# Performance work log

Measured on AMD Instinct MI355X. Metric: run time of the kernel, lower is better.

Reference implementation:

```python
import jax, jax.numpy as jnp
import numpy as np

DELTA = 0.5  # fuzziness factor (module default)

def setup_inputs() -> dict:
    key = jax.random.key(0)
    kq, kk, kv = jax.random.split(key, 3)
    B, L, H, E = 2, 2048, 16, 64
    queries = jax.random.normal(kq, (B, L, H, E), jnp.float32)
    keys_ = jax.random.normal(kk, (B, L, H, E), jnp.float32)
    values = jax.random.normal(kv, (B, L, H, E), jnp.float32)
    # TriangularCausalMask: True above the diagonal -> masked out
    attn_mask = jnp.triu(jnp.ones((L, L), dtype=bool), k=1)[None, None]  # [1,1,L,L]
    return {"queries": queries, "keys": keys_, "values": values, "attn_mask": attn_mask}

def reference(queries, keys, values, attn_mask):
    # queries: [B,L,H,E], keys/values: [B,S,H,E], attn_mask: [1,1,L,S] bool (True = masked)
    E = queries.shape[-1]
    scale = 1.0 / np.sqrt(E)
    scores = jnp.einsum('blhe,bshe->bhls', queries, keys)  # [B,H,L,S]
    # fuzzy modification; note sigmoid(-inf)=0 so masking before or after is equivalent,
    # we mask after for grad safety
    fuzzy = scores + DELTA * jax.nn.sigmoid(scores)
    fuzzy = jnp.where(attn_mask, -jnp.inf, fuzzy)
    A = jax.nn.softmax(scale * fuzzy, axis=-1)  # dropout p=0 (eval mode)
    V = jnp.einsum('bhls,bshd->blhd', A, values)  # [B,L,H,D]
    return V
```

## Files before the change

### kernel.cpp

```cpp
#include <hip/hip_runtime.h>
#include <math.h>


typedef __bf16 bf16x8 __attribute__((ext_vector_type(8)));
typedef __bf16 bf16x4 __attribute__((ext_vector_type(4)));
typedef float  f32x4  __attribute__((ext_vector_type(4)));

constexpr int Lc = 2048, Hc = 16, Ec = 64;
constexpr int QBLK = 64, KVB = 64;
constexpr int NQT  = Lc / QBLK;
constexpr int ROWS = Hc * Ec;
constexpr float LOG2E = 1.4426950408889634f;
constexpr float C1 = 0.125f * LOG2E;
constexpr float C3 = 0.5f * 0.125f * LOG2E;

__global__ __launch_bounds__(256)
void conv_kv(const float* __restrict__ Kp, const float* __restrict__ Vp,
             __bf16* __restrict__ Kbf, __bf16* __restrict__ Vbf) {
    const int bid = blockIdx.x;
    const int tid = threadIdx.x;
    if (bid < 1024) {
        const int task = bid * 256 + tid;
        const int row = task >> 2, q4 = task & 3;
        const int h = row & 15, bl = row >> 4;
        const int b = bl >> 11, l = bl & 2047;
        const float4* src = reinterpret_cast<const float4*>(Kp + (size_t)row * 64 + q4 * 16);
        __bf16* dst = Kbf + ((size_t)((b * 16 + h) * 2048 + l)) * 64 + q4 * 16;
        float4 x0 = src[0], x1 = src[1], x2 = src[2], x3 = src[3];
        bf16x8 o0, o1;
        o0[0]=(__bf16)x0.x; o0[1]=(__bf16)x0.y; o0[2]=(__bf16)x0.z; o0[3]=(__bf16)x0.w;
        o0[4]=(__bf16)x1.x; o0[5]=(__bf16)x1.y; o0[6]=(__bf16)x1.z; o0[7]=(__bf16)x1.w;
        o1[0]=(__bf16)x2.x; o1[1]=(__bf16)x2.y; o1[2]=(__bf16)x2.z; o1[3]=(__bf16)x2.w;
        o1[4]=(__bf16)x3.x; o1[5]=(__bf16)x3.y; o1[6]=(__bf16)x3.z; o1[7]=(__bf16)x3.w;
        reinterpret_cast<bf16x8*>(dst)[0] = o0;
        reinterpret_cast<bf16x8*>(dst)[1] = o1;
    } else {
        __shared__ __bf16 tl[64 * 72];
        const int vb = bid - 1024;
        const int bh = vb >> 5, lt = vb & 31;
        const int b = bh >> 4, h = bh & 15;
        {
            const int l = tid >> 2, dc = tid & 3;
            const float4* src = reinterpret_cast<const float4*>(
                Vp + ((size_t)((b * 2048 + lt * 64 + l) * 16 + h)) * 64 + dc * 16);
            float4 v0 = src[0], v1 = src[1], v2 = src[2], v3 = src[3];
            float e[16] = {v0.x,v0.y,v0.z,v0.w, v1.x,v1.y,v1.z,v1.w,
                           v2.x,v2.y,v2.z,v2.w, v3.x,v3.y,v3.z,v3.w};
            #pragma unroll
            for (int i = 0; i < 16; ++i) tl[(dc * 16 + i) * 72 + l] = (__bf16)e[i];
        }
        __syncthreads();
        {
            const int d = tid >> 2, lc = tid & 3;
            bf16x8 a = *reinterpret_cast<const bf16x8*>(&tl[d * 72 + lc * 16]);
            bf16x8 c = *reinterpret_cast<const bf16x8*>(&tl[d * 72 + lc * 16 + 8]);
            __bf16* dst = Vbf + ((size_t)bh * 64 + d) * 2048 + lt * 64 + lc * 16;
            reinterpret_cast<bf16x8*>(dst)[0] = a;
            reinterpret_cast<bf16x8*>(dst)[1] = c;
        }
    }
}

__global__ __launch_bounds__(256, 4)
void fuzzy_attn_mfma(const float* __restrict__ Qp, const __bf16* __restrict__ Kbf,
                     const __bf16* __restrict__ Vbf, float* __restrict__ Op) {
    __shared__ char smem[24576];
    __bf16* kt0 = reinterpret_cast<__bf16*>(smem);
    __bf16* vt0 = reinterpret_cast<__bf16*>(smem + 8192);

    const int id  = blockIdx.x;
    const int xcd = id & 7;
    const int r_  = id >> 3;
    const int s4  = r_ & 3;
    const int j   = r_ >> 2;
    const int jHi = j >> 3, jLo = j & 7;
    int qt;
    if      (jHi == 0) qt = 31 - jLo;
    else if (jHi == 1) qt = jLo;
    else if (jHi == 2) qt = 23 - jLo;
    else               qt = 8 + jLo;
    const int bh  = s4 * 8 + xcd;
    const int b = bh >> 4, h = bh & 15;

    const int tid  = threadIdx.x;
    const int lane = tid & 63;
    const int w    = tid >> 6;
    const int q16  = lane & 15;
    const int g    = lane >> 4;
    const int qhalf  = w & 1;
    const int kvhalf = w >> 1;

    const __bf16* Kh = Kbf + (size_t)bh * (Lc * Ec);
    const __bf16* Vh = Vbf + (size_t)bh * (Ec * Lc);
    const float*  Qb = Qp + (size_t)b * Lc * ROWS + h * Ec;
    float*        Ob = Op + (size_t)b * Lc * ROWS + h * Ec;

    const int qrow0 = qt * QBLK + qhalf * 32 + q16;
    const int qrow1 = qrow0 + 16;

    const int srow0 = w * 8 + (lane >> 3);
    const int srow1 = srow0 + 32;
    const int sch0  = (lane & 7) ^ ((srow0 & 7) ^ (srow0 >> 3));
    const int sch1  = (lane & 7) ^ ((srow1 & 7) ^ (srow1 >> 3));
    const __bf16* kgA = Kh + srow0 * 64   + sch0 * 8;
    const __bf16* kgB = Kh + srow1 * 64   + sch1 * 8;
    const __bf16* vgA = Vh + srow0 * 2048 + sch0 * 8;
    const __bf16* vgB = Vh + srow1 * 2048 + sch1 * 8;

    bf16x8 qb[2][2];
    #pragma unroll
    for (int qs = 0; qs < 2; ++qs) {
        #pragma unroll
        for (int ks = 0; ks < 2; ++ks) {
            const float* qp = Qb + (size_t)(qs ? qrow1 : qrow0) * ROWS + g * 8 + 32 * ks;
            float4 x0 = reinterpret_cast<const float4*>(qp)[0];
            float4 x1 = reinterpret_cast<const float4*>(qp)[1];
            bf16x8 tq;
            tq[0]=(__bf16)x0.x; tq[1]=(__bf16)x0.y; tq[2]=(__bf16)x0.z; tq[3]=(__bf16)x0.w;
            tq[4]=(__bf16)x1.x; tq[5]=(__bf16)x1.y; tq[6]=(__bf16)x1.z; tq[7]=(__bf16)x1.w;
            qb[qs][ks] = tq;
        }
    }

    const int nst = qt + 1;

    #define STAGE_K(st_)                                                              \
        do {                                                                          \
            const __bf16* kga = kgA + (size_t)(st_) * (KVB * Ec);                     \
            const __bf16* kgb = kgB + (size_t)(st_) * (KVB * Ec);                     \
            __builtin_amdgcn_global_load_lds(                                         \
                (const __attribute__((address_space(1))) void*)kga,                   \
                (__attribute__((address_space(3))) void*)&kt0[w * 512], 16, 0, 0);    \
            __builtin_amdgcn_global_load_lds(                                         \
                (const __attribute__((address_space(1))) void*)kgb,                   \
                (__attribute__((address_space(3))) void*)&kt0[2048 + w * 512], 16, 0, 0); \
        } while (0)
    #define STAGE_V(st_)                                                              \
        do {                                                                          \
            const __bf16* vga = vgA + (st_) * KVB;                                    \
            const __bf16* vgb = vgB + (st_) * KVB;                                    \
            __builtin_amdgcn_global_load_lds(                                         \
                (const __attribute__((address_space(1))) void*)vga,                   \
                (__attribute__((address_space(3))) void*)&vt0[w * 512], 16, 0, 0);    \
            __builtin_amdgcn_global_load_lds(                                         \
                (const __attribute__((address_space(1))) void*)vgb,                   \
                (__attribute__((address_space(3))) void*)&vt0[2048 + w * 512], 16, 0, 0); \
        } while (0)

    STAGE_K(0);
    __syncthreads();

    float la0 = 0.f, la1 = 0.f;
    float lb0 = 0.f, lb1 = 0.f;
    f32x4 oacc[2][4];
    #pragma unroll
    for (int qs = 0; qs < 2; ++qs) {
        #pragma unroll
        for (int ds = 0; ds < 4; ++ds) { f32x4 z = {0.f,0.f,0.f,0.f}; oacc[qs][ds] = z; }
    }

    char* pw = smem + 16384 + w * 2048;
    const int pswz = (q16 & 3) ^ ((q16 >> 2) & 3);

    const char* kbase = reinterpret_cast<const char*>(kt0);
    const char* vbase = reinterpret_cast<const char*>(vt0);

    for (int st = 0; st < nst; ++st) {
        STAGE_V(st);

        f32x4 sacc[2][2];
        #pragma unroll
        for (int kv = 0; kv < 2; ++kv) {
            #pragma unroll
            for (int qs = 0; qs < 2; ++qs) { f32x4 z = {0.f,0.f,0.f,0.f}; sacc[kv][qs] = z; }
        }
        __builtin_amdgcn_s_setprio(1);
        #pragma unroll
        for (int kv = 0; kv < 2; ++kv) {
            const int kvr  = kvhalf * 32 + kv * 16 + q16;
            const int kkey = ((kvr & 7) ^ (kvr >> 3)) << 4;
            #pragma unroll
            for (int ks = 0; ks < 2; ++ks) {
                bf16x8 ka = *reinterpret_cast<const bf16x8*>(
                    kbase + kvr * 128 + (((g + 4 * ks) << 4) ^ kkey));
                sacc[kv][0] = __builtin_amdgcn_mfma_f32_16x16x32_bf16(ka, qb[0][ks], sacc[kv][0], 0, 0, 0);
                sacc[kv][1] = __builtin_amdgcn_mfma_f32_16x16x32_bf16(ka, qb[1][ks], sacc[kv][1], 0, 0, 0);
            }
        }
        __builtin_amdgcn_s_setprio(0);

        const bool diagm = (st == qt) && (kvhalf >= qhalf);
        #pragma unroll
        for (int kv = 0; kv < 2; ++kv) {
            #pragma unroll
            for (int qs = 0; qs < 2; ++qs) {
                const int qrow_s = qs ? qrow1 : qrow0;
                float p4[4];
                #pragma unroll
                for (int r = 0; r < 4; ++r) {
                    const float s  = sacc[kv][qs][r];
                    const float sg = __builtin_amdgcn_fmed3f(fmaf(s, 0.1875f, 0.5f), 0.f, 1.f);
                    float u = fmaf(sg, C3, s * C1);
                    if (diagm) {
                        const int kvg = st * KVB + kvhalf * 32 + kv * 16 + 4 * g + r;
                        if (kvg > qrow_s) u = -INFINITY;
                    }
                    p4[r] = __builtin_amdgcn_exp2f(u);
                }
                if (qs == 0) { la0 += p4[0] + p4[1]; la1 += p4[2] + p4[3]; }
                else         { lb0 += p4[0] + p4[1]; lb1 += p4[2] + p4[3]; }
                bf16x4 pk;
                pk[0]=(__bf16)p4[0]; pk[1]=(__bf16)p4[1]; pk[2]=(__bf16)p4[2]; pk[3]=(__bf16)p4[3];
                *reinterpret_cast<bf16x4*>(
                    pw + (qs * 16 + q16) * 64 +
                    (((2 * kv + (g >> 1)) ^ pswz) << 4) + (g & 1) * 8) = pk;
            }
        }

        __syncthreads();

        if (st + 1 < nst) STAGE_K(st + 1);

        bf16x8 pa0 = *reinterpret_cast<const bf16x8*>(
            pw + (0 * 16 + q16) * 64 + ((g ^ pswz) << 4));
        bf16x8 pa1 = *reinterpret_cast<const bf16x8*>(
            pw + (1 * 16 + q16) * 64 + ((g ^ pswz) << 4));
        __builtin_amdgcn_s_setprio(1);
        #pragma unroll
        for (int ds = 0; ds < 4; ++ds) {
            const int vrow = ds * 16 + q16;
            const int vkey = ((vrow & 7) ^ (vrow >> 3)) << 4;
            bf16x8 vb = *reinterpret_cast<const bf16x8*>(
                vbase + vrow * 128 + (((kvhalf * 4 + g) << 4) ^ vkey));
            oacc[0][ds] = __builtin_amdgcn_mfma_f32_16x16x32_bf16(pa0, vb, oacc[0][ds], 0, 0, 0);
            oacc[1][ds] = __builtin_amdgcn_mfma_f32_16x16x32_bf16(pa1, vb, oacc[1][ds], 0, 0, 0);
        }
        __builtin_amdgcn_s_setprio(0);

        __syncthreads();
    }
    #undef STAGE_K
    #undef STAGE_V

    float lr0 = la0 + la1;
    float lr1 = lb0 + lb1;
    lr0 += __shfl_xor(lr0, 16); lr0 += __shfl_xor(lr0, 32);
    lr1 += __shfl_xor(lr1, 16); lr1 += __shfl_xor(lr1, 32);

    float* sc = reinterpret_cast<float*>(smem);
    float* ls = reinterpret_cast<float*>(smem + 16384);

    if (kvhalf == 1) {
        #pragma unroll
        for (int qs = 0; qs < 2; ++qs) {
            #pragma unroll
            for (int ds = 0; ds < 4; ++ds) {
                #pragma unroll
                for (int r = 0; r < 4; ++r) {
                    sc[qhalf * 2048 + (qs * 16 + g * 4 + r) * 64 + ds * 16 + q16] =
                        oacc[qs][ds][r];
                }
            }
        }
    }
    if (lane < 16) {
        ls[(qhalf * 2 + kvhalf) * 32 + q16]      = lr0;
        ls[(qhalf * 2 + kvhalf) * 32 + 16 + q16] = lr1;
    }
    __syncthreads();

    if (kvhalf == 0) {
        const float inv0 = 1.f / (lr0 + ls[(qhalf * 2 + 1) * 32 + q16]);
        const float inv1 = 1.f / (lr1 + ls[(qhalf * 2 + 1) * 32 + 16 + q16]);
        float i40[4], i41[4];
        #pragma unroll
        for (int r = 0; r < 4; ++r) { i40[r] = __shfl(inv0, g * 4 + r);
                                      i41[r] = __shfl(inv1, g * 4 + r); }
        #pragma unroll
        for (int qs = 0; qs < 2; ++qs) {
            #pragma unroll
            for (int ds = 0; ds < 4; ++ds) {
                #pragma unroll
                for (int r = 0; r < 4; ++r) {
                    const int qlocal = qs * 16 + g * 4 + r;
                    const int row = qt * QBLK + qhalf * 32 + qlocal;
                    const float o = oacc[qs][ds][r] +
                        sc[qhalf * 2048 + qlocal * 64 + ds * 16 + q16];
                    const float sv = qs ? i41[r] : i40[r];
                    Ob[(size_t)row * ROWS + ds * 16 + q16] = o * sv;
                }
            }
        }
    }
}

extern "C" void kernel_launch(void* const* d_in, const int* in_sizes, int n_in,
                              void* d_out, int out_size, void* d_ws, size_t ws_size,
                              hipStream_t stream) {
    (void)in_sizes; (void)n_in; (void)out_size; (void)ws_size;
    const float* Q = (const float*)d_in[0];
    const float* K = (const float*)d_in[1];
    const float* V = (const float*)d_in[2];
    float* O = (float*)d_out;

    __bf16* Kbf = (__bf16*)d_ws;
    __bf16* Vbf = (__bf16*)((char*)d_ws + (size_t)32 * 2048 * 64 * 2);

    conv_kv<<<dim3(2048), dim3(256), 0, stream>>>(K, V, Kbf, Vbf);
    fuzzy_attn_mfma<<<dim3(1024), dim3(256), 0, stream>>>(Q, Kbf, Vbf, O);
}
```

Baseline: 48.09 us.

## Double-buffer K/V tiles and pass P via lane shuffles instead of LDS

```diff
diff --git a/kernel.cpp b/kernel.cpp
--- a/kernel.cpp
+++ b/kernel.cpp
@@ -3,7 +3,7 @@
 
 
 typedef __bf16 bf16x8 __attribute__((ext_vector_type(8)));
-typedef __bf16 bf16x4 __attribute__((ext_vector_type(4)));
+typedef __bf16 bf16x2 __attribute__((ext_vector_type(2)));
 typedef float  f32x4  __attribute__((ext_vector_type(4)));
 
 constexpr int Lc = 2048, Hc = 16, Ec = 64;
@@ -61,12 +61,17 @@
     }
 }
 
+__device__ __forceinline__ unsigned int pk2(float a, float b) {
+    bf16x2 w; w[0] = (__bf16)a; w[1] = (__bf16)b;
+    return __builtin_bit_cast(unsigned int, w);
+}
+
 __global__ __launch_bounds__(256, 4)
 void fuzzy_attn_mfma(const float* __restrict__ Qp, const __bf16* __restrict__ Kbf,
                      const __bf16* __restrict__ Vbf, float* __restrict__ Op) {
-    __shared__ char smem[24576];
+    __shared__ char smem[32768];
     __bf16* kt0 = reinterpret_cast<__bf16*>(smem);
-    __bf16* vt0 = reinterpret_cast<__bf16*>(smem + 8192);
+    __bf16* vt0 = reinterpret_cast<__bf16*>(smem + 16384);
 
     const int id  = blockIdx.x;
     const int xcd = id & 7;
@@ -124,30 +129,31 @@
 
     const int nst = qt + 1;
 
-    #define STAGE_K(st_)                                                              \
+    #define STAGE_K(bufi, st_)                                                        \
         do {                                                                          \
             const __bf16* kga = kgA + (size_t)(st_) * (KVB * Ec);                     \
             const __bf16* kgb = kgB + (size_t)(st_) * (KVB * Ec);                     \
             __builtin_amdgcn_global_load_lds(                                         \
                 (const __attribute__((address_space(1))) void*)kga,                   \
-                (__attribute__((address_space(3))) void*)&kt0[w * 512], 16, 0, 0);    \
+                (__attribute__((address_space(3))) void*)&kt0[(bufi) * 4096 + w * 512], 16, 0, 0); \
             __builtin_amdgcn_global_load_lds(                                         \
                 (const __attribute__((address_space(1))) void*)kgb,                   \
-                (__attribute__((address_space(3))) void*)&kt0[2048 + w * 512], 16, 0, 0); \
+                (__attribute__((address_space(3))) void*)&kt0[(bufi) * 4096 + 2048 + w * 512], 16, 0, 0); \
         } while (0)
-    #define STAGE_V(st_)                                                              \
+    #define STAGE_V(bufi, st_)                                                        \
         do {                                                                          \
             const __bf16* vga = vgA + (st_) * KVB;                                    \
             const __bf16* vgb = vgB + (st_) * KVB;                                    \
             __builtin_amdgcn_global_load_lds(                                         \
                 (const __attribute__((address_space(1))) void*)vga,                   \
-                (__attribute__((address_space(3))) void*)&vt0[w * 512], 16, 0, 0);    \
+                (__attribute__((address_space(3))) void*)&vt0[(bufi) * 4096 + w * 512], 16, 0, 0); \
             __builtin_amdgcn_global_load_lds(                                         \
                 (const __attribute__((address_space(1))) void*)vgb,                   \
-                (__attribute__((address_space(3))) void*)&vt0[2048 + w * 512], 16, 0, 0); \
+                (__attribute__((address_space(3))) void*)&vt0[(bufi) * 4096 + 2048 + w * 512], 16, 0, 0); \
         } while (0)
 
-    STAGE_K(0);
+    STAGE_K(0, 0);
+    STAGE_V(0, 0);
     __syncthreads();
 
     float la0 = 0.f, la1 = 0.f;
@@ -159,14 +165,19 @@
         for (int ds = 0; ds < 4; ++ds) { f32x4 z = {0.f,0.f,0.f,0.f}; oacc[qs][ds] = z; }
     }
 
-    char* pw = smem + 16384 + w * 2048;
-    const int pswz = (q16 & 3) ^ ((q16 >> 2) & 3);
-
-    const char* kbase = reinterpret_cast<const char*>(kt0);
-    const char* vbase = reinterpret_cast<const char*>(vt0);
+    const int shsrc0 = ((2 * g) & 3) * 16 + q16;
+    const int shsrc1 = ((2 * g + 1) & 3) * 16 + q16;
+    const bool hiQ = (g >= 2);
 
     for (int st = 0; st < nst; ++st) {
-        STAGE_V(st);
+        const int buf = st & 1;
+        if (st + 1 < nst) {
+            STAGE_K(buf ^ 1, st + 1);
+            STAGE_V(buf ^ 1, st + 1);
+        }
+
+        const char* kbase = reinterpret_cast<const char*>(kt0 + buf * 4096);
+        const char* vbase = reinterpret_cast<const char*>(vt0 + buf * 4096);
 
         f32x4 sacc[2][2];
         #pragma unroll
@@ -190,12 +201,13 @@
         __builtin_amdgcn_s_setprio(0);
 
         const bool diagm = (st == qt) && (kvhalf >= qhalf);
-        #pragma unroll
-        for (int kv = 0; kv < 2; ++kv) {
-            #pragma unroll
-            for (int qs = 0; qs < 2; ++qs) {
-                const int qrow_s = qs ? qrow1 : qrow0;
-                float p4[4];
+        bf16x8 paf[2];
+        #pragma unroll
+        for (int qs = 0; qs < 2; ++qs) {
+            const int qrow_s = qs ? qrow1 : qrow0;
+            float p0[4], p1[4];
+            #pragma unroll
+            for (int kv = 0; kv < 2; ++kv) {
                 #pragma unroll
                 for (int r = 0; r < 4; ++r) {
                     const float s  = sacc[kv][qs][r];
@@ -205,26 +217,29 @@
                         const int kvg = st * KVB + kvhalf * 32 + kv * 16 + 4 * g + r;
                         if (kvg > qrow_s) u = -INFINITY;
                     }
-                    p4[r] = __builtin_amdgcn_exp2f(u);
+                    const float pv = __builtin_amdgcn_exp2f(u);
+                    if (kv == 0) p0[r] = pv; else p1[r] = pv;
                 }
-                if (qs == 0) { la0 += p4[0] + p4[1]; la1 += p4[2] + p4[3]; }
-                else         { lb0 += p4[0] + p4[1]; lb1 += p4[2] + p4[3]; }
-                bf16x4 pk;
-                pk[0]=(__bf16)p4[0]; pk[1]=(__bf16)p4[1]; pk[2]=(__bf16)p4[2]; pk[3]=(__bf16)p4[3];
-                *reinterpret_cast<bf16x4*>(
-                    pw + (qs * 16 + q16) * 64 +
-                    (((2 * kv + (g >> 1)) ^ pswz) << 4) + (g & 1) * 8) = pk;
             }
-        }
-
-        __syncthreads();
-
-        if (st + 1 < nst) STAGE_K(st + 1);
-
-        bf16x8 pa0 = *reinterpret_cast<const bf16x8*>(
-            pw + (0 * 16 + q16) * 64 + ((g ^ pswz) << 4));
-        bf16x8 pa1 = *reinterpret_cast<const bf16x8*>(
-            pw + (1 * 16 + q16) * 64 + ((g ^ pswz) << 4));
+            if (qs == 0) { la0 += (p0[0] + p0[1]) + (p0[2] + p0[3]);
+                           la1 += (p1[0] + p1[1]) + (p1[2] + p1[3]); }
+            else         { lb0 += (p0[0] + p0[1]) + (p0[2] + p0[3]);
+                           lb1 += (p1[0] + p1[1]) + (p1[2] + p1[3]); }
+
+            const unsigned int w0a = pk2(p0[0], p0[1]), w0b = pk2(p0[2], p0[3]);
+            const unsigned int w1a = pk2(p1[0], p1[1]), w1b = pk2(p1[2], p1[3]);
+            const unsigned int a0 = __shfl((int)w0a, shsrc0), b0 = __shfl((int)w1a, shsrc0);
+            const unsigned int a1 = __shfl((int)w0b, shsrc0), b1 = __shfl((int)w1b, shsrc0);
+            const unsigned int a2 = __shfl((int)w0a, shsrc1), b2 = __shfl((int)w1a, shsrc1);
+            const unsigned int a3 = __shfl((int)w0b, shsrc1), b3 = __shfl((int)w1b, shsrc1);
+            union { unsigned int u[4]; bf16x8 v; } U;
+            U.u[0] = hiQ ? b0 : a0;
+            U.u[1] = hiQ ? b1 : a1;
+            U.u[2] = hiQ ? b2 : a2;
+            U.u[3] = hiQ ? b3 : a3;
+            paf[qs] = U.v;
+        }
+
         __builtin_amdgcn_s_setprio(1);
         #pragma unroll
         for (int ds = 0; ds < 4; ++ds) {
@@ -232,8 +247,8 @@
             const int vkey = ((vrow & 7) ^ (vrow >> 3)) << 4;
             bf16x8 vb = *reinterpret_cast<const bf16x8*>(
                 vbase + vrow * 128 + (((kvhalf * 4 + g) << 4) ^ vkey));
-            oacc[0][ds] = __builtin_amdgcn_mfma_f32_16x16x32_bf16(pa0, vb, oacc[0][ds], 0, 0, 0);
-            oacc[1][ds] = __builtin_amdgcn_mfma_f32_16x16x32_bf16(pa1, vb, oacc[1][ds], 0, 0, 0);
+            oacc[0][ds] = __builtin_amdgcn_mfma_f32_16x16x32_bf16(paf[0], vb, oacc[0][ds], 0, 0, 0);
+            oacc[1][ds] = __builtin_amdgcn_mfma_f32_16x16x32_bf16(paf[1], vb, oacc[1][ds], 0, 0, 0);
         }
         __builtin_amdgcn_s_setprio(0);
 
```

Result: slower. 52.35 us (+8.9%).
